# Kernel optimization log

Measured on AMD Instinct MI355X. Metric: run time of the kernel, lower is better.

## Reference

```python
import jax, jax.numpy as jnp
import numpy as np

NUM_HEADS = 16
MODEL_DIM = 1024
DEPTH = MODEL_DIM // NUM_HEADS
B, S = 4, 1024


def setup_inputs() -> dict:
    key = jax.random.key(0)
    ks = jax.random.split(key, 12)
    sc = 1.0 / np.sqrt(MODEL_DIM)
    q = jax.random.normal(ks[0], (B, S, MODEL_DIM), jnp.float32)
    k = jax.random.normal(ks[1], (B, S, MODEL_DIM), jnp.float32)
    v = jax.random.normal(ks[2], (B, S, MODEL_DIM), jnp.float32)
    # binary padding mask, 1 = masked position (added as mask * -1e9)
    mask = (jax.random.uniform(ks[3], (B, 1, 1, S)) < 0.1).astype(jnp.float32)
    Wq = jax.random.normal(ks[4], (MODEL_DIM, MODEL_DIM), jnp.float32) * sc
    bq = jnp.zeros((MODEL_DIM,), jnp.float32)
    Wk = jax.random.normal(ks[5], (MODEL_DIM, MODEL_DIM), jnp.float32) * sc
    bk = jnp.zeros((MODEL_DIM,), jnp.float32)
    Wv = jax.random.normal(ks[6], (MODEL_DIM, MODEL_DIM), jnp.float32) * sc
    bv = jnp.zeros((MODEL_DIM,), jnp.float32)
    Wo = jax.random.normal(ks[7], (MODEL_DIM, MODEL_DIM), jnp.float32) * sc
    bo = jnp.zeros((MODEL_DIM,), jnp.float32)
    return dict(q=q, k=k, v=v, mask=mask, Wq=Wq, bq=bq, Wk=Wk, bk=bk,
                Wv=Wv, bv=bv, Wo=Wo, bo=bo)


def _split_head(x):
    b, s, _ = x.shape
    return x.reshape(b, s, NUM_HEADS, DEPTH).transpose(0, 2, 1, 3)


def reference(q, k, v, mask, Wq, bq, Wk, bk, Wv, bv, Wo, bo):
    Q = _split_head(q @ Wq + bq)   # (B,H,S,depth)
    K = _split_head(k @ Wk + bk)
    V = _split_head(v @ Wv + bv)
    # NOTE: original divides by k_dim (depth), NOT sqrt(depth) -- keep faithful
    logits = jnp.einsum('bhqd,bhkd->bhqk', Q, K) / jnp.float32(DEPTH)
    logits = logits + mask * (-1e9)
    attn = jax.nn.softmax(logits, axis=-1)         # (B,H,Sq,Sk)
    ctx = jnp.einsum('bhqk,bhkd->bhqd', attn, V)   # (B,H,S,depth)
    ctx = ctx.transpose(0, 2, 1, 3).reshape(q.shape[0], -1, MODEL_DIM)
    out = ctx @ Wo + bo
    return out, attn
```

## Files before the change

kernel.cpp:

```cpp
#include <hip/hip_runtime.h>
#include <stdint.h>
#include <stddef.h>

#define DEV __device__ __forceinline__

typedef __bf16 bf16_t;
typedef bf16_t bf16x8 __attribute__((ext_vector_type(8)));
typedef float f32x4 __attribute__((ext_vector_type(4)));
typedef unsigned short us4 __attribute__((ext_vector_type(4)));
typedef unsigned short us8 __attribute__((ext_vector_type(8)));

DEV float bf2f(unsigned short u) {
    union { unsigned int i; float f; } w; w.i = ((unsigned int)u) << 16; return w.f;
}
DEV unsigned short f2bf(float f) {
    union { unsigned int i; float f; } w; w.f = f;
    unsigned int u = w.i;
    return (unsigned short)((u + 0x7fffu + ((u >> 16) & 1u)) >> 16);
}

DEV void gl_lds16(const void* g, void* l) {
    __builtin_amdgcn_global_load_lds((const __attribute__((address_space(1))) void*)g,
                                     (__attribute__((address_space(3))) void*)l,
                                     16, 0, 0);
}

__global__ void __launch_bounds__(256)
cvt3(const float* __restrict__ s0, const float* __restrict__ s1, const float* __restrict__ s2,
     unsigned short* __restrict__ d0, unsigned short* __restrict__ d1, unsigned short* __restrict__ d2) {
    const float* src    = (blockIdx.z == 0) ? s0 : (blockIdx.z == 1) ? s1 : s2;
    unsigned short* dst = (blockIdx.z == 0) ? d0 : (blockIdx.z == 1) ? d1 : d2;
    int idx = (blockIdx.x * 256 + threadIdx.x) * 4;
    f32x4 v = *(const f32x4*)&src[idx];
    us4 o;
#pragma unroll
    for (int i = 0; i < 4; i++) o[i] = f2bf(v[i]);
    *(us4*)&dst[idx] = o;
}

__global__ void __launch_bounds__(256)
transpose_w(const float* __restrict__ W0, const float* __restrict__ W1,
            const float* __restrict__ W2, const float* __restrict__ W3,
            unsigned short* __restrict__ T0, unsigned short* __restrict__ T1,
            unsigned short* __restrict__ T2, unsigned short* __restrict__ T3) {
    const float* W    = (blockIdx.z == 0) ? W0 : (blockIdx.z == 1) ? W1 : (blockIdx.z == 2) ? W2 : W3;
    unsigned short* T = (blockIdx.z == 0) ? T0 : (blockIdx.z == 1) ? T1 : (blockIdx.z == 2) ? T2 : T3;
    __shared__ float t[32][33];
    int tx = threadIdx.x, ty = threadIdx.y;
    int k0 = blockIdx.x * 32, n0 = blockIdx.y * 32;
#pragma unroll
    for (int r = 0; r < 4; r++)
        t[ty + r * 8][tx] = W[(size_t)(k0 + ty + r * 8) * 1024 + n0 + tx];
    __syncthreads();
#pragma unroll
    for (int r = 0; r < 4; r++)
        T[(size_t)(n0 + ty + r * 8) * 1024 + k0 + tx] = f2bf(t[tx][ty + r * 8]);
}

__global__ void __launch_bounds__(256)
qkv_gemm(const unsigned short* __restrict__ Aq, const unsigned short* __restrict__ Ak,
         const unsigned short* __restrict__ Av,
         const unsigned short* __restrict__ BtQ, const unsigned short* __restrict__ BtK,
         const unsigned short* __restrict__ BtV,
         const float* __restrict__ biq, const float* __restrict__ bik,
         const float* __restrict__ biv,
         unsigned short* __restrict__ Qw, unsigned short* __restrict__ Kw,
         unsigned short* __restrict__ Vtw) {
    const int K = 1024;
    const unsigned short* A  = (blockIdx.z == 0) ? Aq  : (blockIdx.z == 1) ? Ak  : Av;
    const unsigned short* Bt = (blockIdx.z == 0) ? BtQ : (blockIdx.z == 1) ? BtK : BtV;
    const float* bias        = (blockIdx.z == 0) ? biq : (blockIdx.z == 1) ? bik : biv;
    unsigned short* Cout     = (blockIdx.z == 0) ? Qw  : (blockIdx.z == 1) ? Kw  : Vtw;
    const bool vmode = (blockIdx.z == 2);

    __shared__ __align__(16) unsigned short As[128 * 32];
    __shared__ __align__(16) unsigned short Bs[128 * 32];
    int tid = threadIdx.x, lane = tid & 63, wid = tid >> 6;
    int mBase = blockIdx.x * 128, nBase = blockIdx.y * 128;
    int wm = (wid >> 1) * 64, wn = (wid & 1) * 64;
    int c0 = lane & 15, quad = lane >> 4;

    f32x4 acc[4][4] = {};

    for (int k0 = 0; k0 < K; k0 += 32) {
        __syncthreads();
#pragma unroll
        for (int i = 0; i < 2; i++) {
            int cb = wid * 64 + 256 * i;
            int cc = cb + lane;
            int row = cc >> 2, kc = cc & 3;
            gl_lds16(A  + (size_t)(mBase + row) * K + k0 + kc * 8, &As[cb * 8]);
            gl_lds16(Bt + (size_t)(nBase + row) * K + k0 + kc * 8, &Bs[cb * 8]);
        }
        __syncthreads();
        bf16x8 af[4], bfr[4];
#pragma unroll
        for (int t = 0; t < 4; t++) {
            af[t]  = *(const bf16x8*)&As[(wm + t * 16 + c0) * 32 + quad * 8];
            bfr[t] = *(const bf16x8*)&Bs[(wn + t * 16 + c0) * 32 + quad * 8];
        }
#pragma unroll
        for (int mt = 0; mt < 4; mt++)
#pragma unroll
            for (int nt = 0; nt < 4; nt++)
                acc[mt][nt] = __builtin_amdgcn_mfma_f32_16x16x32_bf16(af[mt], bfr[nt], acc[mt][nt], 0, 0, 0);
    }

#pragma unroll
    for (int mt = 0; mt < 4; mt++) {
#pragma unroll
        for (int nt = 0; nt < 4; nt++) {
            int n = nBase + wn + nt * 16 + c0;
            float bv = bias[n];
            if (vmode) {
                int m0 = mBase + wm + mt * 16 + quad * 4;
                int b = m0 >> 10, s = m0 & 1023, h = n >> 6, d = n & 63;
                us4 pk;
#pragma unroll
                for (int r = 0; r < 4; r++) pk[r] = f2bf(acc[mt][nt][r] + bv);
                *(us4*)&Cout[((size_t)((b * 16 + h) * 64 + d)) * 1024 + s] = pk;
            } else {
#pragma unroll
                for (int r = 0; r < 4; r++) {
                    int m = mBase + wm + mt * 16 + quad * 4 + r;
                    int b = m >> 10, s = m & 1023, h = n >> 6, d = n & 63;
                    Cout[((size_t)((b * 16 + h) * 1024 + s)) * 64 + d] = f2bf(acc[mt][nt][r] + bv);
                }
            }
        }
    }
}

__global__ void __launch_bounds__(256)
out_gemm(const unsigned short* __restrict__ A,
         const unsigned short* __restrict__ Bt,
         const float* __restrict__ bias,
         float* __restrict__ Cout) {
    const int K = 1024;
    __shared__ __align__(16) unsigned short As[128 * 32];
    __shared__ __align__(16) unsigned short Bs[128 * 32];
    int tid = threadIdx.x, lane = tid & 63, wid = tid >> 6;
    int mBase = blockIdx.x * 128, nBase = blockIdx.y * 128;
    int wm = (wid >> 1) * 64, wn = (wid & 1) * 64;
    int c0 = lane & 15, quad = lane >> 4;

    f32x4 acc[4][4] = {};

    for (int k0 = 0; k0 < K; k0 += 32) {
        __syncthreads();
#pragma unroll
        for (int i = 0; i < 2; i++) {
            int cb = wid * 64 + 256 * i;
            int cc = cb + lane;
            int row = cc >> 2, kc = cc & 3;
            gl_lds16(A  + (size_t)(mBase + row) * K + k0 + kc * 8, &As[cb * 8]);
            gl_lds16(Bt + (size_t)(nBase + row) * K + k0 + kc * 8, &Bs[cb * 8]);
        }
        __syncthreads();
        bf16x8 af[4], bfr[4];
#pragma unroll
        for (int t = 0; t < 4; t++) {
            af[t]  = *(const bf16x8*)&As[(wm + t * 16 + c0) * 32 + quad * 8];
            bfr[t] = *(const bf16x8*)&Bs[(wn + t * 16 + c0) * 32 + quad * 8];
        }
#pragma unroll
        for (int mt = 0; mt < 4; mt++)
#pragma unroll
            for (int nt = 0; nt < 4; nt++)
                acc[mt][nt] = __builtin_amdgcn_mfma_f32_16x16x32_bf16(af[mt], bfr[nt], acc[mt][nt], 0, 0, 0);
    }
#pragma unroll
    for (int mt = 0; mt < 4; mt++)
#pragma unroll
        for (int nt = 0; nt < 4; nt++) {
            int n = nBase + wn + nt * 16 + c0;
            float bv = bias[n];
#pragma unroll
            for (int r = 0; r < 4; r++) {
                int m = mBase + wm + mt * 16 + quad * 4 + r;
                Cout[(size_t)m * 1024 + n] = acc[mt][nt][r] + bv;
            }
        }
}

__global__ void __launch_bounds__(256, 3)
attn_pv(const unsigned short* __restrict__ Qws,
        const unsigned short* __restrict__ Kws,
        const unsigned short* __restrict__ Vtw,
        const float* __restrict__ maskp,
        float* __restrict__ attnOut,
        unsigned short* __restrict__ ctx) {
    __shared__ __align__(16) unsigned short ldsP[17408];
    __shared__ float redbuf[4][16];

    int tid = threadIdx.x, lane = tid & 63, wid = tid >> 6;
    int c0 = lane & 15, quad = lane >> 4;
    int bh = blockIdx.y, b = bh >> 4, h = bh & 15;
    int q0 = blockIdx.x * 16;

    bf16x8 aq0, aq1;
    {
        const unsigned short* qp = Qws + ((size_t)bh * 1024 + q0 + c0) * 64 + quad * 8;
        aq0 = *(const bf16x8*)qp;
        aq1 = *(const bf16x8*)(qp + 32);
    }

    f32x4 acc[16] = {};

    const unsigned short* kbase = Kws + (size_t)bh * 1024 * 64;
#pragma unroll
    for (int ch = 0; ch < 4; ch++) {
#pragma unroll
        for (int nt = 0; nt < 4; nt++) {
            int srow = ch * 256 + wid * 64 + nt * 16 + c0;
            const unsigned short* kp = kbase + (size_t)srow * 64 + quad * 8;
            bf16x8 b0 = *(const bf16x8*)kp;
            bf16x8 b1 = *(const bf16x8*)(kp + 32);
            int ai = ch * 4 + nt;
            acc[ai] = __builtin_amdgcn_mfma_f32_16x16x32_bf16(aq0, b0, acc[ai], 0, 0, 0);
            acc[ai] = __builtin_amdgcn_mfma_f32_16x16x32_bf16(aq1, b1, acc[ai], 0, 0, 0);
        }
    }

    float lmax[4] = {-3e38f, -3e38f, -3e38f, -3e38f};
#pragma unroll
    for (int i = 0; i < 16; i++) {
        int col = (i >> 2) * 256 + wid * 64 + (i & 3) * 16 + c0;
        float mval = maskp[b * 1024 + col] * (-1e9f);
#pragma unroll
        for (int r = 0; r < 4; r++) {
            float v = acc[i][r] * (1.0f / 64.0f) + mval;
            acc[i][r] = v;
            lmax[r] = fmaxf(lmax[r], v);
        }
    }
#pragma unroll
    for (int st = 1; st < 16; st <<= 1) {
#pragma unroll
        for (int r = 0; r < 4; r++) lmax[r] = fmaxf(lmax[r], __shfl_xor(lmax[r], st, 64));
    }
    if (c0 == 0) {
#pragma unroll
        for (int r = 0; r < 4; r++) redbuf[wid][quad * 4 + r] = lmax[r];
    }
    __syncthreads();
    float rmax[4];
#pragma unroll
    for (int r = 0; r < 4; r++) {
        int row = quad * 4 + r;
        rmax[r] = fmaxf(fmaxf(redbuf[0][row], redbuf[1][row]), fmaxf(redbuf[2][row], redbuf[3][row]));
    }
    float lsum[4] = {0.f, 0.f, 0.f, 0.f};
#pragma unroll
    for (int i = 0; i < 16; i++) {
#pragma unroll
        for (int r = 0; r < 4; r++) {
            float e = __expf(acc[i][r] - rmax[r]);
            acc[i][r] = e;
            lsum[r] += e;
        }
    }
#pragma unroll
    for (int st = 1; st < 16; st <<= 1) {
#pragma unroll
        for (int r = 0; r < 4; r++) lsum[r] += __shfl_xor(lsum[r], st, 64);
    }
    __syncthreads();
    if (c0 == 0) {
#pragma unroll
        for (int r = 0; r < 4; r++) redbuf[wid][quad * 4 + r] = lsum[r];
    }
    __syncthreads();
    float rinv[4];
#pragma unroll
    for (int r = 0; r < 4; r++) {
        int row = quad * 4 + r;
        rinv[r] = 1.0f / (redbuf[0][row] + redbuf[1][row] + redbuf[2][row] + redbuf[3][row]);
    }

    size_t gbase = ((size_t)bh * 1024 + q0) * 1024;
#pragma unroll
    for (int i = 0; i < 16; i++) {
        int kk = (i >> 2) * 64 + (i & 3) * 16 + c0;
        int col = (i >> 2) * 256 + wid * 64 + (i & 3) * 16 + c0;
        int kks = kk ^ (quad << 3);
#pragma unroll
        for (int r = 0; r < 4; r++) {
            int row = quad * 4 + r;
            float pv = acc[i][r] * rinv[r];
            __builtin_nontemporal_store(pv, &attnOut[gbase + (size_t)row * 1024 + col]);
            ldsP[wid * 4352 + row * 272 + kks] = f2bf(pv);
        }
    }
    __syncthreads();

    f32x4 ctx0 = {}, ctx1 = {};
    const unsigned short* vbase = Vtw + ((size_t)(bh * 64 + wid * 16 + c0)) * 1024 + quad * 8;
#pragma unroll
    for (int ch = 0; ch < 4; ch++) {
#pragma unroll
        for (int wv = 0; wv < 4; wv++) {
            int kidx0 = (ch * 64 + quad * 8) ^ ((c0 >> 2) << 3);
            int kidx1 = (ch * 64 + 32 + quad * 8) ^ ((c0 >> 2) << 3);
            bf16x8 a0 = *(const bf16x8*)&ldsP[wv * 4352 + c0 * 272 + kidx0];
            bf16x8 a1 = *(const bf16x8*)&ldsP[wv * 4352 + c0 * 272 + kidx1];
            bf16x8 v0 = *(const bf16x8*)&vbase[ch * 256 + wv * 64];
            bf16x8 v1 = *(const bf16x8*)&vbase[ch * 256 + wv * 64 + 32];
            ctx0 = __builtin_amdgcn_mfma_f32_16x16x32_bf16(a0, v0, ctx0, 0, 0, 0);
            ctx1 = __builtin_amdgcn_mfma_f32_16x16x32_bf16(a1, v1, ctx1, 0, 0, 0);
        }
    }
    f32x4 ctxacc = ctx0 + ctx1;

#pragma unroll
    for (int r = 0; r < 4; r++) {
        int s = q0 + quad * 4 + r;
        ctx[((size_t)(b * 1024 + s)) * 1024 + h * 64 + wid * 16 + c0] = f2bf(ctxacc[r]);
    }
}

extern "C" void kernel_launch(void* const* d_in, const int* in_sizes, int n_in,
                              void* d_out, int out_size, void* d_ws, size_t ws_size,
                              hipStream_t stream) {
    (void)in_sizes; (void)n_in; (void)out_size; (void)ws_size;
    const float* q    = (const float*)d_in[0];
    const float* k    = (const float*)d_in[1];
    const float* v    = (const float*)d_in[2];
    const float* mask = (const float*)d_in[3];
    const float* Wq   = (const float*)d_in[4];
    const float* bq   = (const float*)d_in[5];
    const float* Wk   = (const float*)d_in[6];
    const float* bk   = (const float*)d_in[7];
    const float* Wv   = (const float*)d_in[8];
    const float* bv   = (const float*)d_in[9];
    const float* Wo   = (const float*)d_in[10];
    const float* bo   = (const float*)d_in[11];

    float* outF  = (float*)d_out;
    float* attnF = outF + (size_t)4 * 1024 * 1024;

    unsigned short* wsu = (unsigned short*)d_ws;
    const size_t M1 = (size_t)1024 * 1024;
    unsigned short* WqT = wsu + 0 * M1;
    unsigned short* WkT = wsu + 1 * M1;
    unsigned short* WvT = wsu + 2 * M1;
    unsigned short* WoT = wsu + 3 * M1;
    unsigned short* tq  = wsu + 4 * M1;
    unsigned short* tk  = wsu + 8 * M1;
    unsigned short* tv  = wsu + 12 * M1;
    unsigned short* Qw  = wsu + 16 * M1;
    unsigned short* Kw  = wsu + 20 * M1;
    unsigned short* Vtw = wsu + 24 * M1;
    unsigned short* ctx = wsu + 28 * M1;

    transpose_w<<<dim3(32, 32, 4), dim3(32, 8), 0, stream>>>(Wq, Wk, Wv, Wo, WqT, WkT, WvT, WoT);

    cvt3<<<dim3(4096, 1, 3), 256, 0, stream>>>(q, k, v, tq, tk, tv);

    qkv_gemm<<<dim3(32, 8, 3), 256, 0, stream>>>(tq, tk, tv, WqT, WkT, WvT, bq, bk, bv, Qw, Kw, Vtw);

    attn_pv<<<dim3(64, 64), 256, 0, stream>>>(Qw, Kw, Vtw, mask, attnF, ctx);

    out_gemm<<<dim3(32, 8), 256, 0, stream>>>(ctx, WoT, bo, outF);
}
```

Before: 521.9 us.

## Stage K tiles through LDS, prefetch V fragments, use regular attn stores

Stages each 256-row K chunk into LDS with async global-to-LDS loads before the QK^T MFMAs, replacing direct per-lane global fragment loads. It also prefetches V fragments one chunk ahead in registers so they overlap the PV MFMAs, and turns the nontemporal attention-matrix stores into ordinary stores. The extra barriers and reuse of the ldsP buffer add synchronisation and register pressure. The K tile is written row-contiguous into LDS without swizzling, so LDS bank conflicts are possible.

New measurement: 494.3 us. 5.3% less time.

```diff
diff --git a/kernel.cpp b/kernel.cpp
--- a/kernel.cpp
+++ b/kernel.cpp
@@ -207,13 +207,20 @@
 
     f32x4 acc[16] = {};
 
-    const unsigned short* kbase = Kws + (size_t)bh * 1024 * 64;
-#pragma unroll
     for (int ch = 0; ch < 4; ch++) {
+        __syncthreads();
+#pragma unroll
+        for (int i = 0; i < 8; i++) {
+            int cb = wid * 64 + 256 * i;
+            int cc = cb + lane;
+            int row = cc >> 3, kc = cc & 7;
+            gl_lds16(Kws + ((size_t)bh * 1024 + ch * 256 + row) * 64 + kc * 8, &ldsP[cb * 8]);
+        }
+        __syncthreads();
 #pragma unroll
         for (int nt = 0; nt < 4; nt++) {
-            int srow = ch * 256 + wid * 64 + nt * 16 + c0;
-            const unsigned short* kp = kbase + (size_t)srow * 64 + quad * 8;
+            int srow = wid * 64 + nt * 16 + c0;
+            const unsigned short* kp = &ldsP[srow * 64 + quad * 8];
             bf16x8 b0 = *(const bf16x8*)kp;
             bf16x8 b1 = *(const bf16x8*)(kp + 32);
             int ai = ch * 4 + nt;
@@ -288,27 +295,37 @@
         for (int r = 0; r < 4; r++) {
             int row = quad * 4 + r;
             float pv = acc[i][r] * rinv[r];
-            __builtin_nontemporal_store(pv, &attnOut[gbase + (size_t)row * 1024 + col]);
+            attnOut[gbase + (size_t)row * 1024 + col] = pv;
             ldsP[wid * 4352 + row * 272 + kks] = f2bf(pv);
         }
     }
+
+    const unsigned short* vbase = Vtw + ((size_t)(bh * 64 + wid * 16 + c0)) * 1024 + quad * 8;
+    bf16x8 vcur[8], vnxt[8];
+#pragma unroll
+    for (int j = 0; j < 8; j++)
+        vcur[j] = *(const bf16x8*)&vbase[(j >> 1) * 64 + (j & 1) * 32];
     __syncthreads();
 
     f32x4 ctx0 = {}, ctx1 = {};
-    const unsigned short* vbase = Vtw + ((size_t)(bh * 64 + wid * 16 + c0)) * 1024 + quad * 8;
 #pragma unroll
     for (int ch = 0; ch < 4; ch++) {
+        if (ch < 3) {
+#pragma unroll
+            for (int j = 0; j < 8; j++)
+                vnxt[j] = *(const bf16x8*)&vbase[(ch + 1) * 256 + (j >> 1) * 64 + (j & 1) * 32];
+        }
 #pragma unroll
         for (int wv = 0; wv < 4; wv++) {
             int kidx0 = (ch * 64 + quad * 8) ^ ((c0 >> 2) << 3);
             int kidx1 = (ch * 64 + 32 + quad * 8) ^ ((c0 >> 2) << 3);
             bf16x8 a0 = *(const bf16x8*)&ldsP[wv * 4352 + c0 * 272 + kidx0];
             bf16x8 a1 = *(const bf16x8*)&ldsP[wv * 4352 + c0 * 272 + kidx1];
-            bf16x8 v0 = *(const bf16x8*)&vbase[ch * 256 + wv * 64];
-            bf16x8 v1 = *(const bf16x8*)&vbase[ch * 256 + wv * 64 + 32];
-            ctx0 = __builtin_amdgcn_mfma_f32_16x16x32_bf16(a0, v0, ctx0, 0, 0, 0);
-            ctx1 = __builtin_amdgcn_mfma_f32_16x16x32_bf16(a1, v1, ctx1, 0, 0, 0);
-        }
+            ctx0 = __builtin_amdgcn_mfma_f32_16x16x32_bf16(a0, vcur[wv * 2 + 0], ctx0, 0, 0, 0);
+            ctx1 = __builtin_amdgcn_mfma_f32_16x16x32_bf16(a1, vcur[wv * 2 + 1], ctx1, 0, 0, 0);
+        }
+#pragma unroll
+        for (int j = 0; j < 8; j++) vcur[j] = vnxt[j];
     }
     f32x4 ctxacc = ctx0 + ctx1;
 
```
